# Optimization experiments

Measured on AMD Instinct MI355X. Metric: run time of the kernel, lower is better.

The kernel has to match this reference:

```python
import jax, jax.numpy as jnp
import numpy as np

B, T = 64, 2048
ENC, DEC = 512, 1024
CONV, K, HID = 32, 31, 256
PAD = (K - 1) // 2


def setup_inputs() -> dict:
    key = jax.random.key(0)
    ks = jax.random.split(key, 10)
    s = 0.05
    enc_output = jax.random.normal(ks[0], (B, T, ENC), jnp.float32)
    dec_state = jax.random.normal(ks[1], (B, DEC), jnp.float32)
    prev = jax.random.uniform(ks[2], (B, T), jnp.float32)
    prev_att_w = prev / jnp.sum(prev, axis=-1, keepdims=True)
    text_len = jax.random.randint(ks[3], (B,), T // 2, T + 1)
    W_enc = jax.random.normal(ks[4], (HID, ENC), jnp.float32) * s
    b_enc = jnp.zeros((HID,), jnp.float32)
    W_dec = jax.random.normal(ks[5], (HID, DEC), jnp.float32) * s
    W_att = jax.random.normal(ks[6], (HID, CONV), jnp.float32) * s
    conv_w = jax.random.normal(ks[7], (CONV, 1, K), jnp.float32) * s  # (out,in,k)
    w_w = jax.random.normal(ks[8], (1, HID), jnp.float32) * s
    w_b = jnp.zeros((1,), jnp.float32)
    return dict(enc_output=enc_output, dec_state=dec_state, prev_att_w=prev_att_w,
                text_len=text_len, W_enc=W_enc, b_enc=b_enc, W_dec=W_dec,
                W_att=W_att, conv_w=conv_w, w_w=w_w, w_b=w_b)


def reference(enc_output, dec_state, prev_att_w, text_len,
              W_enc, b_enc, W_dec, W_att, conv_w, w_w, w_b):
    # pad mask: True where position is beyond the valid length
    mask = jnp.arange(T)[None, :] >= text_len[:, None]              # (B,T) bool

    # processed_memory = fc_enc(enc_output)
    pm = jnp.einsum('btc,hc->bth', enc_output, W_enc) + b_enc       # (B,T,HID)

    # location conv over previous attention weights (same-padding 1D conv)
    conv = jax.lax.conv_general_dilated(
        prev_att_w[:, None, :], conv_w, window_strides=(1,),
        padding=[(PAD, PAD)], dimension_numbers=('NCH', 'OIH', 'NCH'))  # (B,CONV,T)
    att_conv = jnp.einsum('bct,hc->bth', conv, W_att)               # (B,T,HID)

    dec = (dec_state @ W_dec.T)[:, None, :]                         # (B,1,HID)

    energy = jnp.einsum('bth,oh->bto', jnp.tanh(att_conv + pm + dec), w_w)[..., 0] + w_b[0]
    energy = jnp.where(mask, -jnp.inf, energy)                      # masked fill
    att_w = jax.nn.softmax(energy, axis=1)                          # (B,T)
    att_c = jnp.einsum('btc,bt->bc', enc_output, att_w)             # (B,ENC)
    return att_c, att_w
```

## Files before the change

kernel.cpp:

```cpp
#include <hip/hip_runtime.h>
#include <hip/hip_bf16.h>

#define NB   64
#define NT   2048
#define NENC 512
#define NDEC 1024
#define NCONV 32
#define NK   31
#define NHID 256
#define NPAD 15

typedef __attribute__((ext_vector_type(8))) short bf16x8;
typedef __attribute__((ext_vector_type(4))) float f32x4;

#define WS_WSW 0
#define WS_GSW 262144
#define WS_DEC 278528
#define WS_CTX 344064
#define WS_ML  4538368

__device__ __forceinline__ short f2b(float f) {
  unsigned u = __builtin_bit_cast(unsigned, f);
  u += 0x7FFFu + ((u >> 16) & 1u);
  return (short)(u >> 16);
}
__device__ __forceinline__ float blo(unsigned u) {
  return __builtin_bit_cast(float, u << 16);
}
__device__ __forceinline__ float bhi(unsigned u) {
  return __builtin_bit_cast(float, u & 0xFFFF0000u);
}

__global__ __launch_bounds__(256) void prep_kernel(
    const float* __restrict__ W_enc, const float* __restrict__ W_att,
    const float* __restrict__ conv_w, const float* __restrict__ dec_state,
    const float* __restrict__ W_dec, char* __restrict__ ws)
{
  const int tid = threadIdx.x;
  const int blk = blockIdx.x;
  if (blk < 512) {
    int idx = blk * 256 + tid;
    int j = idx & 7, lane = (idx >> 3) & 63;
    int ks = (idx >> 9) & 15, nt = idx >> 13;
    int h = nt * 16 + (lane & 15);
    int k = ks * 32 + (lane >> 4) * 8 + j;
    ((short*)(ws + WS_WSW))[idx] = f2b(W_enc[h * NENC + k]);
  } else if (blk < 544) {
    int idx = (blk - 512) * 256 + tid;
    int j = idx & 7, lane = (idx >> 3) & 63, nt = idx >> 9;
    int h = nt * 16 + (lane & 15);
    int k = (lane >> 4) * 8 + j;
    float v = 0.f;
    if (k < NK) {
      for (int c = 0; c < NCONV; ++c)
        v += W_att[h * NCONV + c] * conv_w[c * NK + k];
    }
    ((short*)(ws + WS_GSW))[idx] = f2b(v);
  } else {
    int idx = (blk - 544) * 256 + tid;
    int bh = idx >> 2, q = idx & 3;
    int h = bh & 255, bb = bh >> 8;
    const float4* ds4 = (const float4*)(dec_state + bb * NDEC + q * 256);
    const float4* wd4 = (const float4*)(W_dec + h * NDEC + q * 256);
    float s = 0.f;
#pragma unroll 8
    for (int d = 0; d < 64; ++d) {
      float4 a = ds4[d], w = wd4[d];
      s += a.x * w.x + a.y * w.y + a.z * w.z + a.w * w.w;
    }
    s += __shfl_xor(s, 1);
    s += __shfl_xor(s, 2);
    if (q == 0) ((float*)(ws + WS_DEC))[bh] = s;
  }
}

__global__ __launch_bounds__(256, 2) void energy_kernel(
    const float* __restrict__ enc, const float* __restrict__ prev,
    const int* __restrict__ text_len, const float* __restrict__ b_enc,
    const float* __restrict__ w_w, const float* __restrict__ w_b,
    char* __restrict__ ws, float* __restrict__ e_out)
{
  const int b = blockIdx.y;
  const int bx = blockIdx.x;
  const int t0 = bx * 64;
  const int len = text_len[b];
  if (t0 >= len) return;

  __shared__ short As[64][512];

  const int tid = threadIdx.x;
  const int wave = tid >> 6, lane = tid & 63;
  const int col = lane & 15, quad = lane >> 4;

  const short* Wsw = (const short*)(ws + WS_WSW);
  const short* Gsw = (const short*)(ws + WS_GSW);
  const float* dec_proj = (const float*)(ws + WS_DEC);

  f32x4 acc[4][4];
  {
    bf16x8 gf[4];
#pragma unroll
    for (int i = 0; i < 4; ++i)
      gf[i] = ((const bf16x8*)Gsw)[(wave * 4 + i) * 64 + lane];
    const float* pb = prev + b * NT;
#pragma unroll
    for (int mt = 0; mt < 4; ++mt) {
      int t = t0 + mt * 16 + col;
      bf16x8 pf;
#pragma unroll
      for (int j = 0; j < 8; ++j) {
        int k = quad * 8 + j;
        int ti = t + k - NPAD;
        float v = (k < NK && ti >= 0 && ti < NT) ? pb[ti] : 0.f;
        pf[j] = f2b(v);
      }
      f32x4 z = {0.f, 0.f, 0.f, 0.f};
#pragma unroll
      for (int i = 0; i < 4; ++i)
        acc[mt][i] = __builtin_amdgcn_mfma_f32_16x16x32_bf16(pf, gf[i], z, 0, 0, 0);
    }
  }

  {
    const float* src = enc + ((size_t)b * NT + t0) * NENC;
#pragma unroll 4
    for (int it = 0; it < 16; ++it) {
      int cidx = it * 256 + tid;
      int row = cidx >> 6;
      int c   = cidx & 63;
      const float4* p = (const float4*)(src + row * NENC + c * 8);
      float4 v0 = p[0], v1 = p[1];
      bf16x8 o;
      o[0] = f2b(v0.x); o[1] = f2b(v0.y); o[2] = f2b(v0.z); o[3] = f2b(v0.w);
      o[4] = f2b(v1.x); o[5] = f2b(v1.y); o[6] = f2b(v1.z); o[7] = f2b(v1.w);
      int csw = c ^ (row & 7);
      *(bf16x8*)(&As[row][csw * 8]) = o;
    }
  }
  __syncthreads();

  bf16x8 bcur[4];
#pragma unroll
  for (int i = 0; i < 4; ++i)
    bcur[i] = ((const bf16x8*)Wsw)[((wave * 4 + i) * 16 + 0) * 64 + lane];
#pragma unroll 2
  for (int ks = 0; ks < 16; ++ks) {
    bf16x8 bnxt[4];
    int ksn = (ks + 1) & 15;
#pragma unroll
    for (int i = 0; i < 4; ++i)
      bnxt[i] = ((const bf16x8*)Wsw)[((wave * 4 + i) * 16 + ksn) * 64 + lane];
#pragma unroll
    for (int mt = 0; mt < 4; ++mt) {
      int row = mt * 16 + col;
      int chunk = (ks * 4 + quad) ^ (row & 7);
      bf16x8 af = *(const bf16x8*)(&As[row][chunk * 8]);
#pragma unroll
      for (int i = 0; i < 4; ++i)
        acc[mt][i] = __builtin_amdgcn_mfma_f32_16x16x32_bf16(af, bcur[i], acc[mt][i], 0, 0, 0);
    }
#pragma unroll
    for (int i = 0; i < 4; ++i) bcur[i] = bnxt[i];
  }

  __syncthreads();
  unsigned sv = ((const unsigned*)As)[tid];
  __syncthreads();

  float* ep = (float*)&As[0][0];
  float* wwp = (float*)&As[0][0];

  const float* dpb = dec_proj + b * NHID;
  float pre[4], wv[4];
#pragma unroll
  for (int i = 0; i < 4; ++i) {
    int h = (wave * 4 + i) * 16 + col;
    pre[i] = dpb[h] + b_enc[h];
    wv[i] = w_w[h];
  }
#pragma unroll
  for (int mt = 0; mt < 4; ++mt) {
#pragma unroll
    for (int r = 0; r < 4; ++r) {
      float s = 0.f;
#pragma unroll
      for (int i = 0; i < 4; ++i) {
        float x = acc[mt][i][r] + pre[i];
        float e2 = __expf(2.f * x);
        s += wv[i] * (1.f - 2.f / (e2 + 1.f));
      }
      s += __shfl_xor(s, 1);
      s += __shfl_xor(s, 2);
      s += __shfl_xor(s, 4);
      s += __shfl_xor(s, 8);
      if (col == 0) ep[wave * 64 + mt * 16 + quad * 4 + r] = s;
    }
  }
  __syncthreads();

  if (tid < 64) {
    float e = ep[tid] + ep[64 + tid] + ep[128 + tid] + ep[192 + tid] + w_b[0];
    e_out[b * NT + t0 + tid] = e;
    float me = (t0 + tid < len) ? e : -3.0e38f;
    float m = me;
#pragma unroll
    for (int o = 1; o < 64; o <<= 1) m = fmaxf(m, __shfl_xor(m, o));
    float w = __expf(me - m);
    wwp[tid] = w;
    float l = w;
#pragma unroll
    for (int o = 1; o < 64; o <<= 1) l += __shfl_xor(l, o);
    if (tid == 0) {
      float* ml = (float*)(ws + WS_ML) + (b * 32 + bx) * 2;
      ml[0] = m; ml[1] = l;
    }
  }
  __syncthreads();

  {
    const int c0 = tid * 2;
    const int chunk = c0 >> 3, oc = c0 & 7;
    float w0 = wwp[0];
    float a0 = w0 * blo(sv);
    float a1 = w0 * bhi(sv);
#pragma unroll 7
    for (int t = 1; t < 64; ++t) {
      float w = wwp[t];
      unsigned u = *(const unsigned*)(&As[t][((chunk ^ (t & 7)) << 3) + oc]);
      a0 += w * blo(u);
      a1 += w * bhi(u);
    }
    float2 st = {a0, a1};
    *(float2*)((float*)(ws + WS_CTX) + (size_t)(b * 32 + bx) * NENC + c0) = st;
  }
}

__global__ __launch_bounds__(256) void finalize_kernel(
    const int* __restrict__ text_len, const char* __restrict__ ws,
    float* __restrict__ d_out)
{
  const int b = blockIdx.x, tid = threadIdx.x;
  const int len = text_len[b];
  const int nv = (len + 63) >> 6;
  __shared__ float sc[32];
  __shared__ float sml[2];

  if (tid < 64) {
    const float* ml = (const float*)(ws + WS_ML) + b * 64;
    float mi = -3.0e38f, li = 0.f;
    if (tid < nv) { mi = ml[tid * 2]; li = ml[tid * 2 + 1]; }
    float m = mi;
#pragma unroll
    for (int o = 1; o < 64; o <<= 1) m = fmaxf(m, __shfl_xor(m, o));
    float e = __expf(mi - m);
    float l = li * e;
#pragma unroll
    for (int o = 1; o < 64; o <<= 1) l += __shfl_xor(l, o);
    if (tid < 32) sc[tid] = e;
    if (tid == 0) { sml[0] = m; sml[1] = l; }
  }
  __syncthreads();
  const float m = sml[0], invl = 1.f / sml[1];

  {
    const float* ctx = (const float*)(ws + WS_CTX) + (size_t)b * 32 * NENC;
    float a0 = 0.f, a1 = 0.f;
    for (int i = 0; i < nv; ++i) {
      float s = sc[i];
      a0 += s * ctx[i * NENC + tid];
      a1 += s * ctx[i * NENC + tid + 256];
    }
    d_out[b * NENC + tid] = a0 * invl;
    d_out[b * NENC + tid + 256] = a1 * invl;
  }

  float* aw = d_out + NB * NENC + b * NT;
#pragma unroll
  for (int j = 0; j < 8; ++j) {
    int t = tid + j * 256;
    float v = 0.f;
    if (t < len) v = __expf(aw[t] - m) * invl;
    aw[t] = v;
  }
}

extern "C" void kernel_launch(void* const* d_in, const int* in_sizes, int n_in,
                              void* d_out, int out_size, void* d_ws, size_t ws_size,
                              hipStream_t stream)
{
  const float* enc      = (const float*)d_in[0];
  const float* dec_st   = (const float*)d_in[1];
  const float* prev     = (const float*)d_in[2];
  const int*   text_len = (const int*)d_in[3];
  const float* W_enc    = (const float*)d_in[4];
  const float* b_enc    = (const float*)d_in[5];
  const float* W_dec    = (const float*)d_in[6];
  const float* W_att    = (const float*)d_in[7];
  const float* conv_w   = (const float*)d_in[8];
  const float* w_w      = (const float*)d_in[9];
  const float* w_b      = (const float*)d_in[10];
  float* out = (float*)d_out;
  char* ws = (char*)d_ws;

  hipLaunchKernelGGL(prep_kernel, dim3(800), dim3(256), 0, stream,
                     W_enc, W_att, conv_w, dec_st, W_dec, ws);
  hipLaunchKernelGGL(energy_kernel, dim3(32, 64), dim3(256), 0, stream,
                     enc, prev, text_len, b_enc, w_w, w_b, ws, out + NB * NENC);
  hipLaunchKernelGGL(finalize_kernel, dim3(64), dim3(256), 0, stream,
                     text_len, ws, out);
}
```

Before: 431.7 us.

## Split enc tile load into halves overlapped with MFMA, fuse finalize via last-block counter

```diff
diff --git a/kernel.cpp b/kernel.cpp
--- a/kernel.cpp
+++ b/kernel.cpp
@@ -18,6 +18,7 @@
 #define WS_DEC 278528
 #define WS_CTX 344064
 #define WS_ML  4538368
+#define WS_CNT 4554752
 
 __device__ __forceinline__ short f2b(float f) {
   unsigned u = __builtin_bit_cast(unsigned, f);
@@ -56,7 +57,7 @@
         v += W_att[h * NCONV + c] * conv_w[c * NK + k];
     }
     ((short*)(ws + WS_GSW))[idx] = f2b(v);
-  } else {
+  } else if (blk < 800) {
     int idx = (blk - 544) * 256 + tid;
     int bh = idx >> 2, q = idx & 3;
     int h = bh & 255, bb = bh >> 8;
@@ -71,6 +72,8 @@
     s += __shfl_xor(s, 1);
     s += __shfl_xor(s, 2);
     if (q == 0) ((float*)(ws + WS_DEC))[bh] = s;
+  } else {
+    if (tid < NB) ((int*)(ws + WS_CNT))[tid] = 0;
   }
 }
 
@@ -78,13 +81,14 @@
     const float* __restrict__ enc, const float* __restrict__ prev,
     const int* __restrict__ text_len, const float* __restrict__ b_enc,
     const float* __restrict__ w_w, const float* __restrict__ w_b,
-    char* __restrict__ ws, float* __restrict__ e_out)
+    char* __restrict__ ws, float* __restrict__ d_out)
 {
   const int b = blockIdx.y;
   const int bx = blockIdx.x;
   const int t0 = bx * 64;
   const int len = text_len[b];
   if (t0 >= len) return;
+  const int nv = (len + 63) >> 6;
 
   __shared__ short As[64][512];
 
@@ -95,6 +99,18 @@
   const short* Wsw = (const short*)(ws + WS_WSW);
   const short* Gsw = (const short*)(ws + WS_GSW);
   const float* dec_proj = (const float*)(ws + WS_DEC);
+  float* e_out = d_out + NB * NENC;
+
+  const float* src = enc + ((size_t)b * NT + t0) * NENC;
+
+  float4 pa[8][2];
+#pragma unroll
+  for (int it = 0; it < 8; ++it) {
+    int cidx = it * 256 + tid;
+    int row = cidx >> 5, c = cidx & 31;
+    const float4* p = (const float4*)(src + row * NENC + c * 8);
+    pa[it][0] = p[0]; pa[it][1] = p[1];
+  }
 
   f32x4 acc[4][4];
   {
@@ -121,30 +137,66 @@
     }
   }
 
-  {
-    const float* src = enc + ((size_t)b * NT + t0) * NENC;
-#pragma unroll 4
-    for (int it = 0; it < 16; ++it) {
-      int cidx = it * 256 + tid;
-      int row = cidx >> 6;
-      int c   = cidx & 63;
-      const float4* p = (const float4*)(src + row * NENC + c * 8);
-      float4 v0 = p[0], v1 = p[1];
-      bf16x8 o;
-      o[0] = f2b(v0.x); o[1] = f2b(v0.y); o[2] = f2b(v0.z); o[3] = f2b(v0.w);
-      o[4] = f2b(v1.x); o[5] = f2b(v1.y); o[6] = f2b(v1.z); o[7] = f2b(v1.w);
-      int csw = c ^ (row & 7);
-      *(bf16x8*)(&As[row][csw * 8]) = o;
-    }
-  }
-  __syncthreads();
+#pragma unroll
+  for (int it = 0; it < 8; ++it) {
+    int cidx = it * 256 + tid;
+    int row = cidx >> 5, c = cidx & 31;
+    float4 v0 = pa[it][0], v1 = pa[it][1];
+    bf16x8 o;
+    o[0] = f2b(v0.x); o[1] = f2b(v0.y); o[2] = f2b(v0.z); o[3] = f2b(v0.w);
+    o[4] = f2b(v1.x); o[5] = f2b(v1.y); o[6] = f2b(v1.z); o[7] = f2b(v1.w);
+    int csw = c ^ (row & 7);
+    *(bf16x8*)(&As[row][csw * 8]) = o;
+  }
+  __syncthreads();
+
+  float4 pb2[8][2];
+#pragma unroll
+  for (int it = 0; it < 8; ++it) {
+    int cidx = it * 256 + tid;
+    int row = cidx >> 5, c = (cidx & 31) + 32;
+    const float4* p = (const float4*)(src + row * NENC + c * 8);
+    pb2[it][0] = p[0]; pb2[it][1] = p[1];
+  }
 
   bf16x8 bcur[4];
 #pragma unroll
   for (int i = 0; i < 4; ++i)
     bcur[i] = ((const bf16x8*)Wsw)[((wave * 4 + i) * 16 + 0) * 64 + lane];
 #pragma unroll 2
-  for (int ks = 0; ks < 16; ++ks) {
+  for (int ks = 0; ks < 8; ++ks) {
+    bf16x8 bnxt[4];
+#pragma unroll
+    for (int i = 0; i < 4; ++i)
+      bnxt[i] = ((const bf16x8*)Wsw)[((wave * 4 + i) * 16 + ks + 1) * 64 + lane];
+#pragma unroll
+    for (int mt = 0; mt < 4; ++mt) {
+      int row = mt * 16 + col;
+      int chunk = (ks * 4 + quad) ^ (row & 7);
+      bf16x8 af = *(const bf16x8*)(&As[row][chunk * 8]);
+#pragma unroll
+      for (int i = 0; i < 4; ++i)
+        acc[mt][i] = __builtin_amdgcn_mfma_f32_16x16x32_bf16(af, bcur[i], acc[mt][i], 0, 0, 0);
+    }
+#pragma unroll
+    for (int i = 0; i < 4; ++i) bcur[i] = bnxt[i];
+  }
+
+#pragma unroll
+  for (int it = 0; it < 8; ++it) {
+    int cidx = it * 256 + tid;
+    int row = cidx >> 5, c = (cidx & 31) + 32;
+    float4 v0 = pb2[it][0], v1 = pb2[it][1];
+    bf16x8 o;
+    o[0] = f2b(v0.x); o[1] = f2b(v0.y); o[2] = f2b(v0.z); o[3] = f2b(v0.w);
+    o[4] = f2b(v1.x); o[5] = f2b(v1.y); o[6] = f2b(v1.z); o[7] = f2b(v1.w);
+    int csw = c ^ (row & 7);
+    *(bf16x8*)(&As[row][csw * 8]) = o;
+  }
+  __syncthreads();
+
+#pragma unroll 2
+  for (int ks = 8; ks < 16; ++ks) {
     bf16x8 bnxt[4];
     int ksn = (ks + 1) & 15;
 #pragma unroll
@@ -233,18 +285,20 @@
     float2 st = {a0, a1};
     *(float2*)((float*)(ws + WS_CTX) + (size_t)(b * 32 + bx) * NENC + c0) = st;
   }
-}
-
-__global__ __launch_bounds__(256) void finalize_kernel(
-    const int* __restrict__ text_len, const char* __restrict__ ws,
-    float* __restrict__ d_out)
-{
-  const int b = blockIdx.x, tid = threadIdx.x;
-  const int len = text_len[b];
-  const int nv = (len + 63) >> 6;
-  __shared__ float sc[32];
-  __shared__ float sml[2];
-
+
+  __syncthreads();
+  int* flg = (int*)&As[0][0];
+  if (tid == 0) {
+    __threadfence();
+    int old = atomicAdd((int*)(ws + WS_CNT) + b, 1);
+    int last = (old == nv - 1) ? 1 : 0;
+    if (last) __threadfence();
+    flg[0] = last;
+  }
+  __syncthreads();
+  if (!flg[0]) return;
+
+  float* fsc = (float*)&As[0][0] + 64;
   if (tid < 64) {
     const float* ml = (const float*)(ws + WS_ML) + b * 64;
     float mi = -3.0e38f, li = 0.f;
@@ -256,17 +310,17 @@
     float l = li * e;
 #pragma unroll
     for (int o = 1; o < 64; o <<= 1) l += __shfl_xor(l, o);
-    if (tid < 32) sc[tid] = e;
-    if (tid == 0) { sml[0] = m; sml[1] = l; }
-  }
-  __syncthreads();
-  const float m = sml[0], invl = 1.f / sml[1];
+    if (tid < 32) fsc[tid] = e;
+    if (tid == 0) { fsc[32] = m; fsc[33] = l; }
+  }
+  __syncthreads();
+  const float m = fsc[32], invl = 1.f / fsc[33];
 
   {
     const float* ctx = (const float*)(ws + WS_CTX) + (size_t)b * 32 * NENC;
     float a0 = 0.f, a1 = 0.f;
     for (int i = 0; i < nv; ++i) {
-      float s = sc[i];
+      float s = fsc[i];
       a0 += s * ctx[i * NENC + tid];
       a1 += s * ctx[i * NENC + tid + 256];
     }
@@ -274,7 +328,7 @@
     d_out[b * NENC + tid + 256] = a1 * invl;
   }
 
-  float* aw = d_out + NB * NENC + b * NT;
+  float* aw = e_out + b * NT;
 #pragma unroll
   for (int j = 0; j < 8; ++j) {
     int t = tid + j * 256;
@@ -302,10 +356,8 @@
   float* out = (float*)d_out;
   char* ws = (char*)d_ws;
 
-  hipLaunchKernelGGL(prep_kernel, dim3(800), dim3(256), 0, stream,
+  hipLaunchKernelGGL(prep_kernel, dim3(801), dim3(256), 0, stream,
                      W_enc, W_att, conv_w, dec_st, W_dec, ws);
   hipLaunchKernelGGL(energy_kernel, dim3(32, 64), dim3(256), 0, stream,
-                     enc, prev, text_len, b_enc, w_w, w_b, ws, out + NB * NENC);
-  hipLaunchKernelGGL(finalize_kernel, dim3(64), dim3(256), 0, stream,
-                     text_len, ws, out);
-}
+                     enc, prev, text_len, b_enc, w_w, w_b, ws, out);
+}
```

Result: slower. 499.8 us (+15.8%).

## Halve energy tile to 32 rows and fuse finalize via last-block atomic counter

Applied to the files above, without the earlier changes.

```diff
diff --git a/kernel.cpp b/kernel.cpp
--- a/kernel.cpp
+++ b/kernel.cpp
@@ -17,7 +17,8 @@
 #define WS_GSW 262144
 #define WS_DEC 278528
 #define WS_CTX 344064
-#define WS_ML  4538368
+#define WS_ML  8732672
+#define WS_CNT 8765440
 
 __device__ __forceinline__ short f2b(float f) {
   unsigned u = __builtin_bit_cast(unsigned, f);
@@ -56,7 +57,7 @@
         v += W_att[h * NCONV + c] * conv_w[c * NK + k];
     }
     ((short*)(ws + WS_GSW))[idx] = f2b(v);
-  } else {
+  } else if (blk < 800) {
     int idx = (blk - 544) * 256 + tid;
     int bh = idx >> 2, q = idx & 3;
     int h = bh & 255, bb = bh >> 8;
@@ -71,22 +72,25 @@
     s += __shfl_xor(s, 1);
     s += __shfl_xor(s, 2);
     if (q == 0) ((float*)(ws + WS_DEC))[bh] = s;
-  }
-}
-
-__global__ __launch_bounds__(256, 2) void energy_kernel(
+  } else {
+    if (tid < NB) ((int*)(ws + WS_CNT))[tid] = 0;
+  }
+}
+
+__global__ __launch_bounds__(256, 4) void energy_kernel(
     const float* __restrict__ enc, const float* __restrict__ prev,
     const int* __restrict__ text_len, const float* __restrict__ b_enc,
     const float* __restrict__ w_w, const float* __restrict__ w_b,
-    char* __restrict__ ws, float* __restrict__ e_out)
+    char* __restrict__ ws, float* __restrict__ d_out)
 {
   const int b = blockIdx.y;
   const int bx = blockIdx.x;
-  const int t0 = bx * 64;
+  const int t0 = bx * 32;
   const int len = text_len[b];
   if (t0 >= len) return;
-
-  __shared__ short As[64][512];
+  const int nv = (len + 31) >> 5;
+
+  __shared__ short As[32][512];
 
   const int tid = threadIdx.x;
   const int wave = tid >> 6, lane = tid & 63;
@@ -95,36 +99,12 @@
   const short* Wsw = (const short*)(ws + WS_WSW);
   const short* Gsw = (const short*)(ws + WS_GSW);
   const float* dec_proj = (const float*)(ws + WS_DEC);
-
-  f32x4 acc[4][4];
-  {
-    bf16x8 gf[4];
-#pragma unroll
-    for (int i = 0; i < 4; ++i)
-      gf[i] = ((const bf16x8*)Gsw)[(wave * 4 + i) * 64 + lane];
-    const float* pb = prev + b * NT;
-#pragma unroll
-    for (int mt = 0; mt < 4; ++mt) {
-      int t = t0 + mt * 16 + col;
-      bf16x8 pf;
-#pragma unroll
-      for (int j = 0; j < 8; ++j) {
-        int k = quad * 8 + j;
-        int ti = t + k - NPAD;
-        float v = (k < NK && ti >= 0 && ti < NT) ? pb[ti] : 0.f;
-        pf[j] = f2b(v);
-      }
-      f32x4 z = {0.f, 0.f, 0.f, 0.f};
-#pragma unroll
-      for (int i = 0; i < 4; ++i)
-        acc[mt][i] = __builtin_amdgcn_mfma_f32_16x16x32_bf16(pf, gf[i], z, 0, 0, 0);
-    }
-  }
+  float* e_out = d_out + NB * NENC;
 
   {
     const float* src = enc + ((size_t)b * NT + t0) * NENC;
 #pragma unroll 4
-    for (int it = 0; it < 16; ++it) {
+    for (int it = 0; it < 8; ++it) {
       int cidx = it * 256 + tid;
       int row = cidx >> 6;
       int c   = cidx & 63;
@@ -137,30 +117,48 @@
       *(bf16x8*)(&As[row][csw * 8]) = o;
     }
   }
-  __syncthreads();
-
-  bf16x8 bcur[4];
-#pragma unroll
-  for (int i = 0; i < 4; ++i)
-    bcur[i] = ((const bf16x8*)Wsw)[((wave * 4 + i) * 16 + 0) * 64 + lane];
+
+  f32x4 acc[2][4];
+  {
+    bf16x8 gf[4];
+#pragma unroll
+    for (int i = 0; i < 4; ++i)
+      gf[i] = ((const bf16x8*)Gsw)[(wave * 4 + i) * 64 + lane];
+    const float* pb = prev + b * NT;
+#pragma unroll
+    for (int mt = 0; mt < 2; ++mt) {
+      int t = t0 + mt * 16 + col;
+      bf16x8 pf;
+#pragma unroll
+      for (int j = 0; j < 8; ++j) {
+        int k = quad * 8 + j;
+        int ti = t + k - NPAD;
+        float v = (k < NK && ti >= 0 && ti < NT) ? pb[ti] : 0.f;
+        pf[j] = f2b(v);
+      }
+      f32x4 z = {0.f, 0.f, 0.f, 0.f};
+#pragma unroll
+      for (int i = 0; i < 4; ++i)
+        acc[mt][i] = __builtin_amdgcn_mfma_f32_16x16x32_bf16(pf, gf[i], z, 0, 0, 0);
+    }
+  }
+  __syncthreads();
+
 #pragma unroll 2
   for (int ks = 0; ks < 16; ++ks) {
-    bf16x8 bnxt[4];
-    int ksn = (ks + 1) & 15;
+    bf16x8 bf[4];
 #pragma unroll
     for (int i = 0; i < 4; ++i)
-      bnxt[i] = ((const bf16x8*)Wsw)[((wave * 4 + i) * 16 + ksn) * 64 + lane];
-#pragma unroll
-    for (int mt = 0; mt < 4; ++mt) {
+      bf[i] = ((const bf16x8*)Wsw)[((wave * 4 + i) * 16 + ks) * 64 + lane];
+#pragma unroll
+    for (int mt = 0; mt < 2; ++mt) {
       int row = mt * 16 + col;
       int chunk = (ks * 4 + quad) ^ (row & 7);
       bf16x8 af = *(const bf16x8*)(&As[row][chunk * 8]);
 #pragma unroll
       for (int i = 0; i < 4; ++i)
-        acc[mt][i] = __builtin_amdgcn_mfma_f32_16x16x32_bf16(af, bcur[i], acc[mt][i], 0, 0, 0);
-    }
-#pragma unroll
-    for (int i = 0; i < 4; ++i) bcur[i] = bnxt[i];
+        acc[mt][i] = __builtin_amdgcn_mfma_f32_16x16x32_bf16(af, bf[i], acc[mt][i], 0, 0, 0);
+    }
   }
 
   __syncthreads();
@@ -179,7 +177,7 @@
     wv[i] = w_w[h];
   }
 #pragma unroll
-  for (int mt = 0; mt < 4; ++mt) {
+  for (int mt = 0; mt < 2; ++mt) {
 #pragma unroll
     for (int r = 0; r < 4; ++r) {
       float s = 0.f;
@@ -193,25 +191,25 @@
       s += __shfl_xor(s, 2);
       s += __shfl_xor(s, 4);
       s += __shfl_xor(s, 8);
-      if (col == 0) ep[wave * 64 + mt * 16 + quad * 4 + r] = s;
-    }
-  }
-  __syncthreads();
-
-  if (tid < 64) {
-    float e = ep[tid] + ep[64 + tid] + ep[128 + tid] + ep[192 + tid] + w_b[0];
+      if (col == 0) ep[wave * 32 + mt * 16 + quad * 4 + r] = s;
+    }
+  }
+  __syncthreads();
+
+  if (tid < 32) {
+    float e = ep[tid] + ep[32 + tid] + ep[64 + tid] + ep[96 + tid] + w_b[0];
     e_out[b * NT + t0 + tid] = e;
     float me = (t0 + tid < len) ? e : -3.0e38f;
     float m = me;
 #pragma unroll
-    for (int o = 1; o < 64; o <<= 1) m = fmaxf(m, __shfl_xor(m, o));
+    for (int o = 1; o < 32; o <<= 1) m = fmaxf(m, __shfl_xor(m, o));
     float w = __expf(me - m);
     wwp[tid] = w;
     float l = w;
 #pragma unroll
-    for (int o = 1; o < 64; o <<= 1) l += __shfl_xor(l, o);
+    for (int o = 1; o < 32; o <<= 1) l += __shfl_xor(l, o);
     if (tid == 0) {
-      float* ml = (float*)(ws + WS_ML) + (b * 32 + bx) * 2;
+      float* ml = (float*)(ws + WS_ML) + (b * 64 + bx) * 2;
       ml[0] = m; ml[1] = l;
     }
   }
@@ -224,29 +222,31 @@
     float a0 = w0 * blo(sv);
     float a1 = w0 * bhi(sv);
 #pragma unroll 7
-    for (int t = 1; t < 64; ++t) {
+    for (int t = 1; t < 32; ++t) {
       float w = wwp[t];
       unsigned u = *(const unsigned*)(&As[t][((chunk ^ (t & 7)) << 3) + oc]);
       a0 += w * blo(u);
       a1 += w * bhi(u);
     }
     float2 st = {a0, a1};
-    *(float2*)((float*)(ws + WS_CTX) + (size_t)(b * 32 + bx) * NENC + c0) = st;
-  }
-}
-
-__global__ __launch_bounds__(256) void finalize_kernel(
-    const int* __restrict__ text_len, const char* __restrict__ ws,
-    float* __restrict__ d_out)
-{
-  const int b = blockIdx.x, tid = threadIdx.x;
-  const int len = text_len[b];
-  const int nv = (len + 63) >> 6;
-  __shared__ float sc[32];
-  __shared__ float sml[2];
-
+    *(float2*)((float*)(ws + WS_CTX) + (size_t)(b * 64 + bx) * NENC + c0) = st;
+  }
+
+  __syncthreads();
+  int* flg = (int*)&As[0][0];
+  if (tid == 0) {
+    __threadfence();
+    int old = atomicAdd((int*)(ws + WS_CNT) + b, 1);
+    int last = (old == nv - 1) ? 1 : 0;
+    if (last) __threadfence();
+    flg[0] = last;
+  }
+  __syncthreads();
+  if (!flg[0]) return;
+
+  float* fsc = (float*)&As[0][0] + 64;
   if (tid < 64) {
-    const float* ml = (const float*)(ws + WS_ML) + b * 64;
+    const float* ml = (const float*)(ws + WS_ML) + b * 128;
     float mi = -3.0e38f, li = 0.f;
     if (tid < nv) { mi = ml[tid * 2]; li = ml[tid * 2 + 1]; }
     float m = mi;
@@ -256,17 +256,17 @@
     float l = li * e;
 #pragma unroll
     for (int o = 1; o < 64; o <<= 1) l += __shfl_xor(l, o);
-    if (tid < 32) sc[tid] = e;
-    if (tid == 0) { sml[0] = m; sml[1] = l; }
-  }
-  __syncthreads();
-  const float m = sml[0], invl = 1.f / sml[1];
+    fsc[tid] = e;
+    if (tid == 0) { fsc[64] = m; fsc[65] = l; }
+  }
+  __syncthreads();
+  const float m = fsc[64], invl = 1.f / fsc[65];
 
   {
-    const float* ctx = (const float*)(ws + WS_CTX) + (size_t)b * 32 * NENC;
+    const float* ctx = (const float*)(ws + WS_CTX) + (size_t)b * 64 * NENC;
     float a0 = 0.f, a1 = 0.f;
     for (int i = 0; i < nv; ++i) {
-      float s = sc[i];
+      float s = fsc[i];
       a0 += s * ctx[i * NENC + tid];
       a1 += s * ctx[i * NENC + tid + 256];
     }
@@ -274,7 +274,7 @@
     d_out[b * NENC + tid + 256] = a1 * invl;
   }
 
-  float* aw = d_out + NB * NENC + b * NT;
+  float* aw = e_out + b * NT;
 #pragma unroll
   for (int j = 0; j < 8; ++j) {
     int t = tid + j * 256;
@@ -302,10 +302,8 @@
   float* out = (float*)d_out;
   char* ws = (char*)d_ws;
 
-  hipLaunchKernelGGL(prep_kernel, dim3(800), dim3(256), 0, stream,
+  hipLaunchKernelGGL(prep_kernel, dim3(801), dim3(256), 0, stream,
                      W_enc, W_att, conv_w, dec_st, W_dec, ws);
-  hipLaunchKernelGGL(energy_kernel, dim3(32, 64), dim3(256), 0, stream,
-                     enc, prev, text_len, b_enc, w_w, w_b, ws, out + NB * NENC);
-  hipLaunchKernelGGL(finalize_kernel, dim3(64), dim3(256), 0, stream,
-                     text_len, ws, out);
-}
+  hipLaunchKernelGGL(energy_kernel, dim3(64, 64), dim3(256), 0, stream,
+                     enc, prev, text_len, b_enc, w_w, w_b, ws, out);
+}
```

New measurement: 571.5 us. +32.4%, slower.
